# Kernel tuning notes

Hardware: AMD Instinct MI355X
Metric: run time of the kernel (lower is better)

Reference implementation:

```python
import jax, jax.numpy as jnp
import numpy as np

B, N, D_MODEL, LAP = 64, 64, 256, 16


def setup_inputs() -> dict:
    key = jax.random.key(0)
    ks = jax.random.split(key, 8)
    adj = jax.random.randint(ks[0], (B, N, N), 0, 2, dtype=jnp.int32)
    node_feats = jax.random.normal(ks[1], (B, N, D_MODEL), dtype=jnp.float32)
    eigvec = jax.random.normal(ks[2], (B, N, LAP), dtype=jnp.float32)
    W_lap = jax.random.normal(ks[3], (LAP, D_MODEL), dtype=jnp.float32) / np.sqrt(LAP)
    W_edge = jax.random.normal(ks[4], (1 + 2 * LAP, D_MODEL), dtype=jnp.float32) / np.sqrt(1 + 2 * LAP)
    b_edge = jax.random.normal(ks[5], (D_MODEL,), dtype=jnp.float32) * 0.02
    type_embed = jax.random.normal(ks[6], (2, D_MODEL), dtype=jnp.float32)
    graph_tok = jax.random.normal(ks[7], (1, 1, D_MODEL), dtype=jnp.float32)
    return {"adj": adj, "node_feats": node_feats, "eigvec": eigvec,
            "W_lap": W_lap, "W_edge": W_edge, "b_edge": b_edge,
            "type_embed": type_embed, "graph_tok": graph_tok}


def reference(adj, node_feats, eigvec, W_lap, W_edge, b_edge, type_embed, graph_tok):
    b, n, _ = adj.shape
    d = graph_tok.shape[-1]
    # node tokens: feats + LapPE projection
    node_tok = node_feats + jnp.einsum('bnl,ld->bnd', eigvec, W_lap)
    # upper-triangular candidate edges (fixed M = n(n-1)/2, jit-friendly)
    iu, ju = jnp.triu_indices(n, k=1)               # [M]
    valid = adj[:, iu, ju] > 0                       # [B, M]
    # stable compaction: valid edges first (matches torch per-graph extraction order)
    order = jnp.argsort(~valid, axis=1, stable=True) # [B, M]
    src = iu[order]                                  # [B, M]
    dst = ju[order]
    valid_sorted = jnp.take_along_axis(valid, order, axis=1)
    Pu = jnp.take_along_axis(eigvec, src[..., None], axis=1)  # [B, M, LAP]
    Pv = jnp.take_along_axis(eigvec, dst[..., None], axis=1)
    m = src.shape[1]
    edge_in = jnp.concatenate([jnp.ones((b, m, 1), eigvec.dtype), Pu, Pv], axis=-1)
    etok = jnp.einsum('bmf,fd->bmd', edge_in, W_edge) + b_edge + type_embed[1]
    etok = jnp.where(valid_sorted[..., None], etok, 0.0)      # zeros at padding
    pad_mask_edges = ~valid_sorted                             # True = padding
    gtok = jnp.broadcast_to(graph_tok, (b, 1, d))
    seq_embeds = jnp.concatenate([gtok, node_tok, etok], axis=1)  # [B, 1+n+M, d]
    pad_mask = jnp.concatenate([jnp.zeros((b, 1 + n), bool), pad_mask_edges], axis=1)
    return seq_embeds, pad_mask
```

## Files before the change

### kernel.cpp

```cpp
#include <hip/hip_runtime.h>

#define B_ 64
#define N_ 64
#define D_ 256
#define LAP_ 16
#define M_ 2016
#define TOK_ 2081

typedef float v4f __attribute__((ext_vector_type(4)));

__device__ __forceinline__ void ij_from_m(int m, int& i, int& j) {
    float fm = (float)m;
    int gi = (int)((127.0f - sqrtf(127.0f * 127.0f - 8.0f * fm)) * 0.5f);
    if (gi < 0) gi = 0;
    if (gi > 62) gi = 62;
    while (gi > 0 && (127 * gi - gi * gi) / 2 > m) gi--;
    while (gi < 62 && (127 * (gi + 1) - (gi + 1) * (gi + 1)) / 2 <= m) gi++;
    i = gi;
    j = gi + 1 + (m - (127 * gi - gi * gi) / 2);
}

__global__ __launch_bounds__(256, 4) void prep_kernel(
    const int*   __restrict__ adj,
    const float* __restrict__ node_feats,
    const float* __restrict__ eigvec,
    const float* __restrict__ W_lap,
    const float* __restrict__ W_edge,
    const float* __restrict__ b_edge,
    const float* __restrict__ type_embed,
    const float* __restrict__ graph_tok,
    float*       __restrict__ out,
    float*       __restrict__ wsf,
    int*         __restrict__ src)
{
    __shared__ float sEig[N_ * LAP_];
    __shared__ unsigned long long sWords[32];
    __shared__ int sPref[32];
    __shared__ int sTotal;

    const int b    = blockIdx.x;
    const int cg   = blockIdx.y;
    const int t    = threadIdx.x;
    const int wave = t >> 6, lane = t & 63;

    ((float4*)sEig)[t] = ((const float4*)(eigvec + (size_t)b * N_ * LAP_))[t];

#pragma unroll
    for (int k = 0; k < 8; k++) {
        int m = k * 256 + t;
        int valid = 0;
        if (m < M_) {
            int i, j;
            ij_from_m(m, i, j);
            valid = (adj[b * (N_ * N_) + i * N_ + j] > 0) ? 1 : 0;
        }
        unsigned long long blt = __ballot(valid);
        if (lane == 0) sWords[k * 4 + wave] = blt;
    }

    const int colS = cg * 64 + lane;
    float w1c[LAP_], w2c[LAP_], wlc[LAP_];
#pragma unroll
    for (int l = 0; l < LAP_; l++) {
        w1c[l] = W_edge[(1 + l) * D_ + colS];
        w2c[l] = W_edge[(1 + LAP_ + l) * D_ + colS];
        wlc[l] = W_lap[l * D_ + t];
    }
    __syncthreads();

    if (t < 32) {
        int cnt = __popcll(sWords[t]);
        int inc = cnt;
#pragma unroll
        for (int off = 1; off < 32; off <<= 1) {
            int v = __shfl_up(inc, off);
            if (lane >= off) inc += v;
        }
        sPref[t] = inc - cnt;
        if (t == 31) sTotal = inc;
    }
    __syncthreads();

    float* Ub = wsf + 256 + (size_t)b * N_ * D_;
    float* Vb = Ub + (size_t)B_ * N_ * D_;
#pragma unroll 2
    for (int n16 = 0; n16 < 16; n16++) {
        int n = wave * 16 + n16;
        const float* e = sEig + n * LAP_;
        float aU = 0.0f, aV = 0.0f;
#pragma unroll
        for (int l = 0; l < LAP_; l++) {
            float el = e[l];
            aU += el * w1c[l];
            aV += el * w2c[l];
        }
        Ub[n * D_ + colS] = aU;
        Vb[n * D_ + colS] = aV;
    }

    float* outB = out + (size_t)b * TOK_ * D_;
#pragma unroll 4
    for (int k = 0; k < 16; k++) {
        int n = cg * 16 + k;
        float a = node_feats[((size_t)b * N_ + n) * D_ + t];
        const float* e = sEig + n * LAP_;
#pragma unroll
        for (int l = 0; l < LAP_; l++) a += e[l] * wlc[l];
        outB[(size_t)(1 + n) * D_ + t] = a;
    }

    const int total = sTotal;
    float* maskb = out + (size_t)B_ * TOK_ * D_ + (size_t)b * TOK_;
    for (int idx = t; idx < 504; idx += 256) {
        int m = cg * 504 + idx;
        int w = m >> 6, r = m & 63;
        unsigned long long word = sWords[w];
        int rank = sPref[w] + __popcll(word & ((1ull << r) - 1ull));
        int valid = (int)((word >> r) & 1ull);
        int p = valid ? rank : total + (m - rank);
        int i, j;
        ij_from_m(m, i, j);
        src[b * M_ + p] = i | (j << 6) | (valid << 12);
        maskb[1 + N_ + p] = valid ? 0.0f : 1.0f;
    }

    if (cg == 0) {
        wsf[t] = W_edge[t] + b_edge[t] + type_embed[D_ + t];
        outB[t] = graph_tok[t];
        if (t < 1 + N_) maskb[t] = 0.0f;
    }
}

__global__ __launch_bounds__(256, 8) void edge_kernel(
    const float* __restrict__ wsf,
    const int*   __restrict__ src,
    float*       __restrict__ out)
{
    const int bid  = blockIdx.x;
    const int xcd  = bid & 7;
    const int idx  = bid >> 3;
    const int b    = ((idx & 7) << 3) | xcd;
    const int s    = idx >> 3;
    const int wave = threadIdx.x >> 6, lane = threadIdx.x & 63;

    v4f base4 = ((const v4f*)wsf)[lane];
    const float* Ub = wsf + 256 + (size_t)b * N_ * D_;
    const float* Vb = Ub + (size_t)B_ * N_ * D_;
    const int* sb = src + b * M_;
    float* outE = out + (size_t)b * TOK_ * D_ + (size_t)(1 + N_) * D_;

    const int p0 = s * 63;
    for (int p = p0 + wave; p < p0 + 63; p += 4) {
        int info = sb[p];
        v4f val = {0.0f, 0.0f, 0.0f, 0.0f};
        if (info & (1 << 12)) {
            int si = info & 63, di = (info >> 6) & 63;
            v4f u = ((const v4f*)(Ub + si * D_))[lane];
            v4f v = ((const v4f*)(Vb + di * D_))[lane];
            val = base4 + u + v;
        }
        ((v4f*)(outE + (size_t)p * D_))[lane] = val;
    }
}

extern "C" void kernel_launch(void* const* d_in, const int* in_sizes, int n_in,
                              void* d_out, int out_size, void* d_ws, size_t ws_size,
                              hipStream_t stream) {
    const int*   adj        = (const int*)d_in[0];
    const float* node_feats = (const float*)d_in[1];
    const float* eigvec     = (const float*)d_in[2];
    const float* W_lap      = (const float*)d_in[3];
    const float* W_edge     = (const float*)d_in[4];
    const float* b_edge     = (const float*)d_in[5];
    const float* type_embed = (const float*)d_in[6];
    const float* graph_tok  = (const float*)d_in[7];
    float* out = (float*)d_out;

    float* wsf = (float*)d_ws;
    int*   src = (int*)(wsf + 256 + 2 * (size_t)B_ * N_ * D_);

    prep_kernel<<<dim3(B_, 4), dim3(256), 0, stream>>>(
        adj, node_feats, eigvec, W_lap, W_edge, b_edge, type_embed, graph_tok,
        out, wsf, src);
    edge_kernel<<<dim3(2048), dim3(256), 0, stream>>>(wsf, src, out);
}
```

Measured before the change: 178.4 us.

## Split prep kernel across eight column groups, stage adjacency in LDS, prefetch edge info

The prep kernel grid doubles from four to eight column groups per graph. Each block now computes only one of the U or V projections and half the node rows, and the launch bound drops to 2 blocks per SM. The whole adjacency matrix is loaded into shared memory with coalesced int4 loads instead of scattered global gathers. In the edge kernel, each wave loads its edge info words in one go and broadcasts them with shuffles instead of issuing a serial load per iteration. Each prep block now reloads the 16 KB adjacency matrix, so adjacency traffic grows, and the extra LDS lowers occupancy.

```diff
diff --git a/kernel.cpp b/kernel.cpp
--- a/kernel.cpp
+++ b/kernel.cpp
@@ -20,7 +20,7 @@
     j = gi + 1 + (m - (127 * gi - gi * gi) / 2);
 }
 
-__global__ __launch_bounds__(256, 4) void prep_kernel(
+__global__ __launch_bounds__(256, 2) void prep_kernel(
     const int*   __restrict__ adj,
     const float* __restrict__ node_feats,
     const float* __restrict__ eigvec,
@@ -33,6 +33,7 @@
     float*       __restrict__ wsf,
     int*         __restrict__ src)
 {
+    __shared__ int   sAdj[N_ * N_];
     __shared__ float sEig[N_ * LAP_];
     __shared__ unsigned long long sWords[32];
     __shared__ int sPref[32];
@@ -43,7 +44,21 @@
     const int t    = threadIdx.x;
     const int wave = t >> 6, lane = t & 63;
 
+#pragma unroll
+    for (int r = 0; r < 4; r++)
+        ((int4*)sAdj)[r * 256 + t] =
+            ((const int4*)(adj + (size_t)b * (N_ * N_)))[r * 256 + t];
     ((float4*)sEig)[t] = ((const float4*)(eigvec + (size_t)b * N_ * LAP_))[t];
+
+    const float* Wsel = (cg < 4) ? (W_edge + D_) : (W_edge + (1 + LAP_) * D_);
+    const int colS = (cg & 3) * 64 + lane;
+    float wc[LAP_], wlc[LAP_];
+#pragma unroll
+    for (int l = 0; l < LAP_; l++) {
+        wc[l]  = Wsel[l * D_ + colS];
+        wlc[l] = W_lap[l * D_ + t];
+    }
+    __syncthreads();
 
 #pragma unroll
     for (int k = 0; k < 8; k++) {
@@ -52,19 +67,10 @@
         if (m < M_) {
             int i, j;
             ij_from_m(m, i, j);
-            valid = (adj[b * (N_ * N_) + i * N_ + j] > 0) ? 1 : 0;
+            valid = (sAdj[i * N_ + j] > 0) ? 1 : 0;
         }
         unsigned long long blt = __ballot(valid);
         if (lane == 0) sWords[k * 4 + wave] = blt;
-    }
-
-    const int colS = cg * 64 + lane;
-    float w1c[LAP_], w2c[LAP_], wlc[LAP_];
-#pragma unroll
-    for (int l = 0; l < LAP_; l++) {
-        w1c[l] = W_edge[(1 + l) * D_ + colS];
-        w2c[l] = W_edge[(1 + LAP_ + l) * D_ + colS];
-        wlc[l] = W_lap[l * D_ + t];
     }
     __syncthreads();
 
@@ -83,25 +89,21 @@
 
     float* Ub = wsf + 256 + (size_t)b * N_ * D_;
     float* Vb = Ub + (size_t)B_ * N_ * D_;
+    float* Tb = (cg < 4) ? Ub : Vb;
 #pragma unroll 2
     for (int n16 = 0; n16 < 16; n16++) {
         int n = wave * 16 + n16;
         const float* e = sEig + n * LAP_;
-        float aU = 0.0f, aV = 0.0f;
+        float acc = 0.0f;
 #pragma unroll
-        for (int l = 0; l < LAP_; l++) {
-            float el = e[l];
-            aU += el * w1c[l];
-            aV += el * w2c[l];
-        }
-        Ub[n * D_ + colS] = aU;
-        Vb[n * D_ + colS] = aV;
+        for (int l = 0; l < LAP_; l++) acc += e[l] * wc[l];
+        Tb[n * D_ + colS] = acc;
     }
 
     float* outB = out + (size_t)b * TOK_ * D_;
 #pragma unroll 4
-    for (int k = 0; k < 16; k++) {
-        int n = cg * 16 + k;
+    for (int k = 0; k < 8; k++) {
+        int n = cg * 8 + k;
         float a = node_feats[((size_t)b * N_ + n) * D_ + t];
         const float* e = sEig + n * LAP_;
 #pragma unroll
@@ -111,17 +113,20 @@
 
     const int total = sTotal;
     float* maskb = out + (size_t)B_ * TOK_ * D_ + (size_t)b * TOK_;
-    for (int idx = t; idx < 504; idx += 256) {
-        int m = cg * 504 + idx;
-        int w = m >> 6, r = m & 63;
-        unsigned long long word = sWords[w];
-        int rank = sPref[w] + __popcll(word & ((1ull << r) - 1ull));
-        int valid = (int)((word >> r) & 1ull);
-        int p = valid ? rank : total + (m - rank);
-        int i, j;
-        ij_from_m(m, i, j);
-        src[b * M_ + p] = i | (j << 6) | (valid << 12);
-        maskb[1 + N_ + p] = valid ? 0.0f : 1.0f;
+    {
+        int idx = t;
+        if (idx < 252) {
+            int m = cg * 252 + idx;
+            int w = m >> 6, r = m & 63;
+            unsigned long long word = sWords[w];
+            int rank = sPref[w] + __popcll(word & ((1ull << r) - 1ull));
+            int valid = (int)((word >> r) & 1ull);
+            int p = valid ? rank : total + (m - rank);
+            int i, j;
+            ij_from_m(m, i, j);
+            src[b * M_ + p] = i | (j << 6) | (valid << 12);
+            maskb[1 + N_ + p] = valid ? 0.0f : 1.0f;
+        }
     }
 
     if (cg == 0) {
@@ -150,8 +155,14 @@
     float* outE = out + (size_t)b * TOK_ * D_ + (size_t)(1 + N_) * D_;
 
     const int p0 = s * 63;
-    for (int p = p0 + wave; p < p0 + 63; p += 4) {
-        int info = sb[p];
+    const int q15 = lane & 15;
+    const int nq  = (63 - wave + 3) >> 2;
+    int myinfo = (wave + 4 * q15 < 63) ? sb[p0 + wave + 4 * q15] : 0;
+
+#pragma unroll 4
+    for (int q = 0; q < nq; q++) {
+        int info = __shfl(myinfo, q);
+        int p = p0 + wave + 4 * q;
         v4f val = {0.0f, 0.0f, 0.0f, 0.0f};
         if (info & (1 << 12)) {
             int si = info & 63, di = (info >> 6) & 63;
@@ -179,7 +190,7 @@
     float* wsf = (float*)d_ws;
     int*   src = (int*)(wsf + 256 + 2 * (size_t)B_ * N_ * D_);
 
-    prep_kernel<<<dim3(B_, 4), dim3(256), 0, stream>>>(
+    prep_kernel<<<dim3(B_, 8), dim3(256), 0, stream>>>(
         adj, node_feats, eigvec, W_lap, W_edge, b_edge, type_embed, graph_tok,
         out, wsf, src);
     edge_kernel<<<dim3(2048), dim3(256), 0, stream>>>(wsf, src, out);
```

New measurement: 167.7 us. 6.0% less time.
